# Optimization experiments

Measured on AMD Instinct MI355X. Metric: run time of the kernel, lower is better.

Reference implementation:

```python
import jax, jax.numpy as jnp
import numpy as np
from jax import lax

B, M = 16384, 128
NUM_LAYERS, OW, OH = 22, 11, 11
MAX_VEC = np.array([9.0, 1.0, 1.0, 10.0, 3.0, 254.0, 1.0, 1.0, 235.0, 8.0, 9.0, 250.0,
                    29.0, 1.0, 1.0, 8.0, 1.0, 1.0, 6.0, 3.0, 1.0, 2.0], dtype=np.float32)


def setup_inputs() -> dict:
    key = jax.random.key(0)
    ks = jax.random.split(key, 20)
    s = 0.05
    return {
        "observations": jax.random.randint(ks[0], (B, M, 3), 0, 255, dtype=jnp.int32),
        "cnn1_w": jax.random.normal(ks[1], (64, 22, 5, 5), jnp.float32) * s,
        "cnn1_b": jnp.zeros((64,), jnp.float32),
        "cnn2_w": jax.random.normal(ks[2], (64, 64, 3, 3), jnp.float32) * s,
        "cnn2_b": jnp.zeros((64,), jnp.float32),
        "fc1_w": jax.random.normal(ks[3], (128, 64), jnp.float32) * s,
        "fc1_b": jnp.zeros((128,), jnp.float32),
        "enc_w": jax.random.normal(ks[4], (128, 128), jnp.float32) * s,
        "enc_b": jnp.zeros((128,), jnp.float32),
        "critic1_w": jax.random.normal(ks[5], (1024, 128), jnp.float32) * s,
        "critic1_b": jnp.zeros((1024,), jnp.float32),
        "value_w": jax.random.normal(ks[6], (1, 1024), jnp.float32) * s,
        "value_b": jnp.zeros((1,), jnp.float32),
        "actor1_w": jax.random.normal(ks[7], (512, 128), jnp.float32) * s,
        "actor1_b": jnp.zeros((512,), jnp.float32),
        "action_emb": jax.random.normal(ks[8], (100, 16), jnp.float32) * s,
        "head0_w": jax.random.normal(ks[9], (9, 528), jnp.float32) * s,
        "head0_b": jnp.zeros((9,), jnp.float32),
        "head1_w": jax.random.normal(ks[10], (10, 528), jnp.float32) * s,
        "head1_b": jnp.zeros((10,), jnp.float32),
    }


def _encode_scatter(observations):
    # zero-out any byte equal to 255 (matches torch in-place masking)
    tok = jnp.where(observations == 255, 0, observations)  # [B, M, 3]
    coords = tok[..., 0].astype(jnp.uint8)
    x = ((coords >> 4) & 15).astype(jnp.int32)
    y = (coords & 15).astype(jnp.int32)
    atr = tok[..., 1].astype(jnp.int32)
    val = tok[..., 2].astype(jnp.float32)
    b, m = atr.shape
    valid = (x < OW) & (y < OH) & (atr < NUM_LAYERS)
    b_idx = jnp.broadcast_to(jnp.arange(b, dtype=jnp.int32)[:, None], (b, m))
    b_idx = jnp.where(valid, b_idx, b)  # route invalid tokens out of bounds -> dropped
    box = jnp.zeros((b, NUM_LAYERS, OW, OH), jnp.float32)
    box = box.at[b_idx, atr, x, y].set(val, mode="drop")
    return box


def _forward(observations, cnn1_w, cnn1_b, cnn2_w, cnn2_b, fc1_w, fc1_b, enc_w, enc_b,
             critic1_w, critic1_b, value_w, value_b, actor1_w, actor1_b, action_emb,
             head0_w, head0_b, head1_w, head1_b):
    box = _encode_scatter(observations)
    x = box / jnp.asarray(MAX_VEC)[None, :, None, None]
    dn = ("NCHW", "OIHW", "NCHW")
    x = lax.conv_general_dilated(x, cnn1_w, (3, 3), "VALID", dimension_numbers=dn) + cnn1_b[None, :, None, None]
    x = lax.conv_general_dilated(x, cnn2_w, (1, 1), "VALID", dimension_numbers=dn) + cnn2_b[None, :, None, None]
    x = x.reshape(x.shape[0], -1)                 # [B, 64]
    x = x @ fc1_w.T + fc1_b                       # [B, 128]
    hidden = x @ enc_w.T + enc_b                  # [B, 128]
    critic = jnp.tanh(hidden @ critic1_w.T + critic1_b)
    value = critic @ value_w.T + value_b          # [B, 1]
    actor = hidden @ actor1_w.T + actor1_b        # [B, 512]
    emb = jnp.broadcast_to(action_emb.mean(axis=0)[None, :], (actor.shape[0], action_emb.shape[1]))
    comb = jnp.concatenate([actor, emb], axis=-1)  # [B, 528]
    logits = jnp.concatenate([comb @ head0_w.T + head0_b, comb @ head1_w.T + head1_b], axis=-1)
    return logits, value


def reference(observations, cnn1_w, cnn1_b, cnn2_w, cnn2_b, fc1_w, fc1_b, enc_w, enc_b,
              critic1_w, critic1_b, value_w, value_b, actor1_w, actor1_b, action_emb,
              head0_w, head0_b, head1_w, head1_b):
    return _forward(observations, cnn1_w, cnn1_b, cnn2_w, cnn2_b, fc1_w, fc1_b, enc_w, enc_b,
                    critic1_w, critic1_b, value_w, value_b, actor1_w, actor1_b, action_emb,
                    head0_w, head0_b, head1_w, head1_b)
```

## Files before the change

### kernel.cpp

```cpp
#include <hip/hip_runtime.h>
#include <math.h>

#define NB 16384
#define NTOK 128
#define NKEY 2662
#define NLOG 19
#define TB 16

typedef __attribute__((ext_vector_type(8))) short short8;
typedef __attribute__((ext_vector_type(4))) float floatx4;

__device__ __constant__ float c_maxv[22] = {
    9.f, 1.f, 1.f, 10.f, 3.f, 254.f, 1.f, 1.f, 235.f, 8.f, 9.f, 250.f,
    29.f, 1.f, 1.f, 8.f, 1.f, 1.f, 6.f, 3.f, 1.f, 2.f};

__device__ __forceinline__ unsigned short f2bf(float f) {
    unsigned u = __float_as_uint(f);
    return (unsigned short)((u + 0x7FFFu + ((u >> 16) & 1u)) >> 16);
}
__device__ __forceinline__ float tanh_fast(float x) {
    float e = __builtin_amdgcn_exp2f(x * 2.885390082f);
    return 1.f - 2.f * __builtin_amdgcn_rcpf(e + 1.f);
}

__global__ __launch_bounds__(256) void k_pre(
    const float* __restrict__ w1, const float* __restrict__ b1,
    const float* __restrict__ w2, const float* __restrict__ b2,
    const float* __restrict__ fc1w, const float* __restrict__ fc1b,
    const float* __restrict__ encw, const float* __restrict__ encb,
    const float* __restrict__ a1w, const float* __restrict__ a1b,
    const float* __restrict__ aemb,
    const float* __restrict__ h0w, const float* __restrict__ h0b,
    const float* __restrict__ h1w, const float* __restrict__ h1b,
    const float* __restrict__ c1w,
    float* __restrict__ G, float* __restrict__ E,
    float* __restrict__ beff, float* __restrict__ Wlog,
    float* __restrict__ blog, unsigned short* __restrict__ c1wb)
{
    __shared__ float s_w2[72 * 65];
    __shared__ float s_h2[64];
    __shared__ float s_t[128];
    __shared__ float s_emb[16];
    const int bid = blockIdx.x, t = threadIdx.x;
    if (bid < 666) {
        const int v = t & 63;
        const int key_u = __builtin_amdgcn_readfirstlane(bid * 4 + (t >> 6));
        const int key_c = (key_u < NKEY) ? key_u : (NKEY - 1);
        const int c = key_c / 121, rem = key_c % 121, X = rem / 11, Y = rem % 11;
        float acc = 0.f;
        for (int u0 = 0; u0 < 64; u0 += 8) {
            __syncthreads();
            #pragma unroll
            for (int r = 0; r < 18; ++r) {
                int g = t + 256 * r;
                int vg = g / 72, rg = g % 72;
                s_w2[rg * 65 + vg] = w2[vg * 576 + u0 * 9 + rg];
            }
            __syncthreads();
            #pragma unroll
            for (int ur = 0; ur < 8; ++ur) {
                const int w1base = (u0 + ur) * 550 + c * 25;
                #pragma unroll
                for (int i = 0; i < 3; ++i) {
                    int xi = X - 3 * i;
                    if (xi < 0 || xi > 4) continue;
                    #pragma unroll
                    for (int j = 0; j < 3; ++j) {
                        int yj = Y - 3 * j;
                        if (yj < 0 || yj > 4) continue;
                        acc += s_w2[(ur * 9 + i * 3 + j) * 65 + v] *
                               w1[w1base + xi * 5 + yj];
                    }
                }
            }
        }
        if (key_u < NKEY) G[key_u * 64 + v] = acc / c_maxv[c];
    } else if (bid < 698) {
        int m = (bid - 666) * 256 + t;
        int h = __builtin_amdgcn_readfirstlane(m >> 6) & 127;
        int v = t & 63;
        float acc = 0.f;
        #pragma unroll 8
        for (int p = 0; p < 128; ++p)
            acc += encw[h * 128 + p] * fc1w[p * 64 + v];
        E[v * 128 + h] = acc;
    } else if (bid == 698) {
        {
            int o = t >> 2, q = t & 3;
            const float* wp = w2 + (o * 64 + q * 16) * 9;
            float s = 0.f;
            #pragma unroll
            for (int ui = 0; ui < 16; ++ui) {
                float ws = 0.f;
                #pragma unroll
                for (int k = 0; k < 9; ++k) ws += wp[ui * 9 + k];
                s += b1[q * 16 + ui] * ws;
            }
            s += __shfl_xor(s, 1, 64);
            s += __shfl_xor(s, 2, 64);
            if (q == 0) s_h2[o] = s + b2[o];
        }
        __syncthreads();
        if (t < 128) {
            const float4* f4 = (const float4*)(fc1w + t * 64);
            float s = fc1b[t];
            #pragma unroll
            for (int vq = 0; vq < 16; ++vq) {
                float4 w = f4[vq];
                s += w.x * s_h2[vq * 4]     + w.y * s_h2[vq * 4 + 1] +
                     w.z * s_h2[vq * 4 + 2] + w.w * s_h2[vq * 4 + 3];
            }
            s_t[t] = s;
        } else if (t < 192) {
            int lane = t & 63;
            int e = lane & 15, rq = lane >> 4;
            float s = 0.f;
            #pragma unroll
            for (int rr = 0; rr < 25; ++rr) s += aemb[(rq * 25 + rr) * 16 + e];
            s += __shfl_xor(s, 16, 64);
            s += __shfl_xor(s, 32, 64);
            if (lane < 16) s_emb[e] = s * 0.01f;
        }
        __syncthreads();
        if (t < 128) {
            const float4* e4 = (const float4*)(encw + t * 128);
            float s = encb[t];
            #pragma unroll
            for (int pq = 0; pq < 32; ++pq) {
                float4 w = e4[pq];
                s += w.x * s_t[pq * 4]     + w.y * s_t[pq * 4 + 1] +
                     w.z * s_t[pq * 4 + 2] + w.w * s_t[pq * 4 + 3];
            }
            beff[t] = s;
        } else {
            int tp = t - 128;
            int os = tp >> 3, ai = tp & 7;
            #pragma unroll
            for (int rep = 0; rep < 2; ++rep) {
                int o = os + rep * 16;
                int oc = (o < NLOG) ? o : (NLOG - 1);
                const float* hw = (oc < 9) ? (h0w + oc * 528)
                                           : (h1w + (oc - 9) * 528);
                float s = 0.f;
                for (int a = ai; a < 528; a += 8) {
                    float m = (a < 512) ? a1b[a] : s_emb[a - 512];
                    s += hw[a] * m;
                }
                s += __shfl_xor(s, 1, 64);
                s += __shfl_xor(s, 2, 64);
                s += __shfl_xor(s, 4, 64);
                if (ai == 0 && o < NLOG)
                    blog[o] = s + ((o < 9) ? h0b[o] : h1b[o - 9]);
            }
        }
    } else if (bid < 709) {
        int n = (bid - 699) * 256 + t;
        if (n < NLOG * 128) {
            int o = __builtin_amdgcn_readfirstlane(n >> 7);
            int h = n & 127;
            const float* hw = (o < 9) ? (h0w + o * 528) : (h1w + (o - 9) * 528);
            float acc = 0.f;
            #pragma unroll 8
            for (int a = 0; a < 512; ++a)
                acc += hw[a] * a1w[a * 128 + h];
            Wlog[n] = acc;
        }
    } else {
        int n = ((bid - 709) * 256 + t) * 8;
        float4 a = *(const float4*)(c1w + n);
        float4 b4 = *(const float4*)(c1w + n + 4);
        short8 r;
        r[0] = (short)f2bf(a.x);  r[1] = (short)f2bf(a.y);
        r[2] = (short)f2bf(a.z);  r[3] = (short)f2bf(a.w);
        r[4] = (short)f2bf(b4.x); r[5] = (short)f2bf(b4.y);
        r[6] = (short)f2bf(b4.z); r[7] = (short)f2bf(b4.w);
        *(short8*)(c1wb + n) = r;
    }
}

__global__ __launch_bounds__(512, 6) void k_main(
    const int* __restrict__ obs,
    const float* __restrict__ G, const float* __restrict__ E,
    const float* __restrict__ beff,
    const unsigned short* __restrict__ c1wb, const float* __restrict__ c1b,
    const float* __restrict__ vw, const float* __restrict__ vb,
    const float* __restrict__ Wlog, const float* __restrict__ blog,
    float* __restrict__ out)
{
    __shared__ int            s_lst[TB * 32];
    __shared__ float          s_hidden[TB * 128];
    __shared__ unsigned short s_hb[TB * 136];
    __shared__ float          s_x[TB * 64];
    __shared__ int            s_cnt[TB];
    __shared__ float          s_val[8 * 16];

    const int tid = threadIdx.x, bid = blockIdx.x;
    const int b0 = bid * TB;

    if (tid < TB) s_cnt[tid] = 0;
    __syncthreads();

    {
        const int4* p = (const int4*)(obs + (size_t)(b0 * NTOK + 4 * tid) * 3);
        int4 A = p[0], Bv = p[1], Cv = p[2];
        int d[12] = {A.x, A.y, A.z, A.w, Bv.x, Bv.y, Bv.z, Bv.w,
                     Cv.x, Cv.y, Cv.z, Cv.w};
        #pragma unroll
        for (int s = 0; s < 4; ++s) {
            int o0 = d[3 * s], o1 = d[3 * s + 1], o2 = d[3 * s + 2];
            o0 = (o0 == 255) ? 0 : o0;
            o1 = (o1 == 255) ? 0 : o1;
            o2 = (o2 == 255) ? 0 : o2;
            int x = (o0 >> 4) & 15, y = o0 & 15;
            if (x < 11 && y < 11 && o1 < 22) {
                int tt = 4 * tid + s;
                int bb = tt >> 7, m = tt & 127;
                int pos = atomicAdd(&s_cnt[bb], 1);
                if (pos < 32)
                    s_lst[bb * 32 + pos] =
                        (m << 20) | (o2 << 12) | (o1 * 121 + x * 11 + y);
            }
        }
    }
    __syncthreads();

    {
        int bb = tid >> 5, e = tid & 31;
        int n = s_cnt[bb]; if (n > 32) n = 32;
        if (e < n) {
            int p = s_lst[bb * 32 + e];
            bool dead = false;
            for (int i = 0; i < n; ++i) {
                int q = s_lst[bb * 32 + i];
                dead |= (((q ^ p) & 0xFFF) == 0) && (q > p);
            }
            if (dead) s_lst[bb * 32 + e] = p & ~0x000FF000;
        }
    }
    __syncthreads();

    {
        int w = tid >> 6, lane = tid & 63;
        int bbA = 2 * w, bbB = 2 * w + 1;
        int nA = s_cnt[bbA]; if (nA > 32) nA = 32;
        int nB = s_cnt[bbB]; if (nB > 32) nB = 32;
        int nm = (nA > nB) ? nA : nB;
        float aA = 0.f, aB = 0.f;
        for (int i = 0; i < nm; ++i) {
            if (i < nA) {
                int p = s_lst[bbA * 32 + i];
                aA += (float)((p >> 12) & 0xFF) * G[(p & 0xFFF) * 64 + lane];
            }
            if (i < nB) {
                int p = s_lst[bbB * 32 + i];
                aB += (float)((p >> 12) & 0xFF) * G[(p & 0xFFF) * 64 + lane];
            }
        }
        s_x[bbA * 64 + lane] = aA;
        s_x[bbB * 64 + lane] = aB;
    }
    __syncthreads();

    {
        int g = tid >> 7, h = tid & 127;
        float be = beff[h];
        float acc[4] = {be, be, be, be};
        const float4* x4 = (const float4*)s_x;
        #pragma unroll
        for (int vq = 0; vq < 16; ++vq) {
            float ev0 = E[(vq * 4 + 0) * 128 + h];
            float ev1 = E[(vq * 4 + 1) * 128 + h];
            float ev2 = E[(vq * 4 + 2) * 128 + h];
            float ev3 = E[(vq * 4 + 3) * 128 + h];
            #pragma unroll
            for (int b = 0; b < 4; ++b) {
                float4 xv = x4[(g * 4 + b) * 16 + vq];
                acc[b] += xv.x * ev0 + xv.y * ev1 + xv.z * ev2 + xv.w * ev3;
            }
        }
        #pragma unroll
        for (int b = 0; b < 4; ++b) {
            int bb = g * 4 + b;
            s_hidden[bb * 128 + h] = acc[b];
            s_hb[bb * 136 + h] = f2bf(acc[b]);
        }
    }
    __syncthreads();

    {
        const int lane = tid & 63, w = tid >> 6;
        const int lm = lane & 15, quad = lane >> 4;
        short8 af[4];
        #pragma unroll
        for (int kk = 0; kk < 4; ++kk)
            af[kk] = *(const short8*)&s_hb[lm * 136 + kk * 32 + quad * 8];
        float vp[4] = {0.f, 0.f, 0.f, 0.f};
        for (int nt = 0; nt < 8; ++nt) {
            int j = w * 128 + nt * 16 + lm;
            const short8* cp = (const short8*)&c1wb[j * 128];
            floatx4 a0 = {0.f, 0.f, 0.f, 0.f};
            #pragma unroll
            for (int kk = 0; kk < 4; ++kk) {
                short8 bf = cp[kk * 4 + quad];
                a0 = __builtin_amdgcn_mfma_f32_16x16x32_bf16(af[kk], bf, a0, 0, 0, 0);
            }
            float bj = c1b[j], wj = vw[j];
            #pragma unroll
            for (int r = 0; r < 4; ++r)
                vp[r] += tanh_fast(a0[r] + bj) * wj;
        }
        #pragma unroll
        for (int off = 1; off <= 8; off <<= 1)
            #pragma unroll
            for (int r = 0; r < 4; ++r)
                vp[r] += __shfl_xor(vp[r], off, 64);
        if (lm == 0) {
            #pragma unroll
            for (int r = 0; r < 4; ++r)
                s_val[w * 16 + quad * 4 + r] = vp[r];
        }
    }

    {
        const float4* s_h4 = (const float4*)s_hidden;
        const float4* wl4  = (const float4*)Wlog;
        int bl = tid >> 5, o = tid & 31;
        if (o < NLOG) {
            float acc = blog[o];
            #pragma unroll
            for (int hq = 0; hq < 32; ++hq) {
                float4 hv = s_h4[bl * 32 + hq];
                float4 wl = wl4[o * 32 + hq];
                acc += wl.x * hv.x + wl.y * hv.y + wl.z * hv.z + wl.w * hv.w;
            }
            out[(b0 + bl) * NLOG + o] = acc;
        }
    }
    __syncthreads();
    if (tid < TB) {
        float v = 0.f;
        #pragma unroll
        for (int w = 0; w < 8; ++w) v += s_val[w * 16 + tid];
        out[NB * NLOG + b0 + tid] = v + vb[0];
    }
}

extern "C" void kernel_launch(void* const* d_in, const int* in_sizes, int n_in,
                              void* d_out, int out_size, void* d_ws, size_t ws_size,
                              hipStream_t stream)
{
    const int*   obs  = (const int*)  d_in[0];
    const float* w1   = (const float*)d_in[1];
    const float* b1   = (const float*)d_in[2];
    const float* w2   = (const float*)d_in[3];
    const float* b2   = (const float*)d_in[4];
    const float* fc1w = (const float*)d_in[5];
    const float* fc1b = (const float*)d_in[6];
    const float* encw = (const float*)d_in[7];
    const float* encb = (const float*)d_in[8];
    const float* c1w  = (const float*)d_in[9];
    const float* c1b  = (const float*)d_in[10];
    const float* vw   = (const float*)d_in[11];
    const float* vb   = (const float*)d_in[12];
    const float* a1w  = (const float*)d_in[13];
    const float* a1b  = (const float*)d_in[14];
    const float* aemb = (const float*)d_in[15];
    const float* h0w  = (const float*)d_in[16];
    const float* h0b  = (const float*)d_in[17];
    const float* h1w  = (const float*)d_in[18];
    const float* h1b  = (const float*)d_in[19];

    float* W    = (float*)d_ws;
    float* G    = W;
    float* E    = W + 170368;
    float* beff = W + 178560;
    float* Wlog = W + 178688;
    float* blog = W + 181120;
    unsigned short* c1wb = (unsigned short*)(W + 181152);

    hipLaunchKernelGGL(k_pre, dim3(773), dim3(256), 0, stream,
                       w1, b1, w2, b2, fc1w, fc1b, encw, encb, a1w, a1b, aemb,
                       h0w, h0b, h1w, h1b, c1w,
                       G, E, beff, Wlog, blog, c1wb);
    hipLaunchKernelGGL(k_main, dim3(NB / TB), dim3(512), 0, stream,
                       obs, G, E, beff, c1wb, c1b, vw, vb, Wlog, blog,
                       (float*)d_out);
}
```

Before: 200.1 us.

## Enlarge main-kernel batch tile to 64 and compute 4 keys per wave in precompute

The main kernel now handles 64 batch rows per block with 1024 threads. Each wave computes four 16-row MFMA tiles against the same bf16 critic weight fragments, so every weight load is reused four times and global weight traffic per row drops. The precompute kernel gives each wave four G keys so the staged conv2 weights in shared memory are reused more, which cuts its block count. The cost is a quarter as many main blocks (256), more registers per thread, and lower occupancy limits.

```diff
diff --git a/kernel.cpp b/kernel.cpp
--- a/kernel.cpp
+++ b/kernel.cpp
@@ -5,7 +5,7 @@
 #define NTOK 128
 #define NKEY 2662
 #define NLOG 19
-#define TB 16
+#define TB 64
 
 typedef __attribute__((ext_vector_type(8))) short short8;
 typedef __attribute__((ext_vector_type(4))) float floatx4;
@@ -42,12 +42,19 @@
     __shared__ float s_t[128];
     __shared__ float s_emb[16];
     const int bid = blockIdx.x, t = threadIdx.x;
-    if (bid < 666) {
+    if (bid < 167) {
         const int v = t & 63;
-        const int key_u = __builtin_amdgcn_readfirstlane(bid * 4 + (t >> 6));
-        const int key_c = (key_u < NKEY) ? key_u : (NKEY - 1);
-        const int c = key_c / 121, rem = key_c % 121, X = rem / 11, Y = rem % 11;
-        float acc = 0.f;
+        const int wv = __builtin_amdgcn_readfirstlane(t >> 6);
+        int c_[4], X_[4], Y_[4];
+        #pragma unroll
+        for (int kk = 0; kk < 4; ++kk) {
+            int key_u = bid * 16 + wv * 4 + kk;
+            int key_c = (key_u < NKEY) ? key_u : (NKEY - 1);
+            c_[kk] = key_c / 121;
+            int rem = key_c % 121;
+            X_[kk] = rem / 11; Y_[kk] = rem % 11;
+        }
+        float acc[4] = {0.f, 0.f, 0.f, 0.f};
         for (int u0 = 0; u0 < 64; u0 += 8) {
             __syncthreads();
             #pragma unroll
@@ -59,24 +66,32 @@
             __syncthreads();
             #pragma unroll
             for (int ur = 0; ur < 8; ++ur) {
-                const int w1base = (u0 + ur) * 550 + c * 25;
                 #pragma unroll
-                for (int i = 0; i < 3; ++i) {
-                    int xi = X - 3 * i;
-                    if (xi < 0 || xi > 4) continue;
+                for (int kk = 0; kk < 4; ++kk) {
+                    const int w1base = (u0 + ur) * 550 + c_[kk] * 25;
                     #pragma unroll
-                    for (int j = 0; j < 3; ++j) {
-                        int yj = Y - 3 * j;
-                        if (yj < 0 || yj > 4) continue;
-                        acc += s_w2[(ur * 9 + i * 3 + j) * 65 + v] *
-                               w1[w1base + xi * 5 + yj];
+                    for (int i = 0; i < 3; ++i) {
+                        int xi = X_[kk] - 3 * i;
+                        if (xi < 0 || xi > 4) continue;
+                        #pragma unroll
+                        for (int j = 0; j < 3; ++j) {
+                            int yj = Y_[kk] - 3 * j;
+                            if (yj < 0 || yj > 4) continue;
+                            acc[kk] += s_w2[(ur * 9 + i * 3 + j) * 65 + v] *
+                                       w1[w1base + xi * 5 + yj];
+                        }
                     }
                 }
             }
         }
-        if (key_u < NKEY) G[key_u * 64 + v] = acc / c_maxv[c];
-    } else if (bid < 698) {
-        int m = (bid - 666) * 256 + t;
+        #pragma unroll
+        for (int kk = 0; kk < 4; ++kk) {
+            int key_u = bid * 16 + wv * 4 + kk;
+            if (key_u < NKEY)
+                G[key_u * 64 + v] = acc[kk] / c_maxv[c_[kk]];
+        }
+    } else if (bid < 199) {
+        int m = (bid - 167) * 256 + t;
         int h = __builtin_amdgcn_readfirstlane(m >> 6) & 127;
         int v = t & 63;
         float acc = 0.f;
@@ -84,7 +99,7 @@
         for (int p = 0; p < 128; ++p)
             acc += encw[h * 128 + p] * fc1w[p * 64 + v];
         E[v * 128 + h] = acc;
-    } else if (bid == 698) {
+    } else if (bid == 199) {
         {
             int o = t >> 2, q = t & 3;
             const float* wp = w2 + (o * 64 + q * 16) * 9;
@@ -153,8 +168,8 @@
                     blog[o] = s + ((o < 9) ? h0b[o] : h1b[o - 9]);
             }
         }
-    } else if (bid < 709) {
-        int n = (bid - 699) * 256 + t;
+    } else if (bid < 210) {
+        int n = (bid - 200) * 256 + t;
         if (n < NLOG * 128) {
             int o = __builtin_amdgcn_readfirstlane(n >> 7);
             int h = n & 127;
@@ -166,7 +181,7 @@
             Wlog[n] = acc;
         }
     } else {
-        int n = ((bid - 709) * 256 + t) * 8;
+        int n = ((bid - 210) * 256 + t) * 8;
         float4 a = *(const float4*)(c1w + n);
         float4 b4 = *(const float4*)(c1w + n + 4);
         short8 r;
@@ -178,7 +193,7 @@
     }
 }
 
-__global__ __launch_bounds__(512, 6) void k_main(
+__global__ __launch_bounds__(1024, 4) void k_main(
     const int* __restrict__ obs,
     const float* __restrict__ G, const float* __restrict__ E,
     const float* __restrict__ beff,
@@ -192,7 +207,7 @@
     __shared__ unsigned short s_hb[TB * 136];
     __shared__ float          s_x[TB * 64];
     __shared__ int            s_cnt[TB];
-    __shared__ float          s_val[8 * 16];
+    __shared__ float          s_val[16 * 64];
 
     const int tid = threadIdx.x, bid = blockIdx.x;
     const int b0 = bid * TB;
@@ -201,70 +216,82 @@
     __syncthreads();
 
     {
-        const int4* p = (const int4*)(obs + (size_t)(b0 * NTOK + 4 * tid) * 3);
-        int4 A = p[0], Bv = p[1], Cv = p[2];
-        int d[12] = {A.x, A.y, A.z, A.w, Bv.x, Bv.y, Bv.z, Bv.w,
-                     Cv.x, Cv.y, Cv.z, Cv.w};
-        #pragma unroll
-        for (int s = 0; s < 4; ++s) {
-            int o0 = d[3 * s], o1 = d[3 * s + 1], o2 = d[3 * s + 2];
-            o0 = (o0 == 255) ? 0 : o0;
-            o1 = (o1 == 255) ? 0 : o1;
-            o2 = (o2 == 255) ? 0 : o2;
-            int x = (o0 >> 4) & 15, y = o0 & 15;
-            if (x < 11 && y < 11 && o1 < 22) {
-                int tt = 4 * tid + s;
-                int bb = tt >> 7, m = tt & 127;
-                int pos = atomicAdd(&s_cnt[bb], 1);
-                if (pos < 32)
-                    s_lst[bb * 32 + pos] =
-                        (m << 20) | (o2 << 12) | (o1 * 121 + x * 11 + y);
-            }
-        }
-    }
-    __syncthreads();
-
-    {
-        int bb = tid >> 5, e = tid & 31;
-        int n = s_cnt[bb]; if (n > 32) n = 32;
-        if (e < n) {
-            int p = s_lst[bb * 32 + e];
-            bool dead = false;
-            for (int i = 0; i < n; ++i) {
-                int q = s_lst[bb * 32 + i];
-                dead |= (((q ^ p) & 0xFFF) == 0) && (q > p);
-            }
-            if (dead) s_lst[bb * 32 + e] = p & ~0x000FF000;
+        const int gtok0 = b0 * NTOK;
+        #pragma unroll
+        for (int k = 0; k < 2; ++k) {
+            int g = tid + 1024 * k;
+            const int4* p = (const int4*)(obs + (size_t)(gtok0 + 4 * g) * 3);
+            int4 A = p[0], Bv = p[1], Cv = p[2];
+            int d[12] = {A.x, A.y, A.z, A.w, Bv.x, Bv.y, Bv.z, Bv.w,
+                         Cv.x, Cv.y, Cv.z, Cv.w};
+            #pragma unroll
+            for (int s = 0; s < 4; ++s) {
+                int o0 = d[3 * s], o1 = d[3 * s + 1], o2 = d[3 * s + 2];
+                o0 = (o0 == 255) ? 0 : o0;
+                o1 = (o1 == 255) ? 0 : o1;
+                o2 = (o2 == 255) ? 0 : o2;
+                int x = (o0 >> 4) & 15, y = o0 & 15;
+                if (x < 11 && y < 11 && o1 < 22) {
+                    int tt = 4 * g + s;
+                    int bb = tt >> 7, m = tt & 127;
+                    int pos = atomicAdd(&s_cnt[bb], 1);
+                    if (pos < 32)
+                        s_lst[bb * 32 + pos] =
+                            (m << 20) | (o2 << 12) | (o1 * 121 + x * 11 + y);
+                }
+            }
+        }
+    }
+    __syncthreads();
+
+    {
+        #pragma unroll
+        for (int rep = 0; rep < 2; ++rep) {
+            int bb = (tid >> 5) + rep * 32, e = tid & 31;
+            int n = s_cnt[bb]; if (n > 32) n = 32;
+            if (e < n) {
+                int p = s_lst[bb * 32 + e];
+                bool dead = false;
+                for (int i = 0; i < n; ++i) {
+                    int q = s_lst[bb * 32 + i];
+                    dead |= (((q ^ p) & 0xFFF) == 0) && (q > p);
+                }
+                if (dead) s_lst[bb * 32 + e] = p & ~0x000FF000;
+            }
         }
     }
     __syncthreads();
 
     {
         int w = tid >> 6, lane = tid & 63;
-        int bbA = 2 * w, bbB = 2 * w + 1;
-        int nA = s_cnt[bbA]; if (nA > 32) nA = 32;
-        int nB = s_cnt[bbB]; if (nB > 32) nB = 32;
-        int nm = (nA > nB) ? nA : nB;
-        float aA = 0.f, aB = 0.f;
+        int n4[4], nm = 0;
+        #pragma unroll
+        for (int q = 0; q < 4; ++q) {
+            int n = s_cnt[w * 4 + q]; if (n > 32) n = 32;
+            n4[q] = n; nm = (n > nm) ? n : nm;
+        }
+        float a4[4] = {0.f, 0.f, 0.f, 0.f};
         for (int i = 0; i < nm; ++i) {
-            if (i < nA) {
-                int p = s_lst[bbA * 32 + i];
-                aA += (float)((p >> 12) & 0xFF) * G[(p & 0xFFF) * 64 + lane];
-            }
-            if (i < nB) {
-                int p = s_lst[bbB * 32 + i];
-                aB += (float)((p >> 12) & 0xFF) * G[(p & 0xFFF) * 64 + lane];
-            }
-        }
-        s_x[bbA * 64 + lane] = aA;
-        s_x[bbB * 64 + lane] = aB;
+            #pragma unroll
+            for (int q = 0; q < 4; ++q) {
+                if (i < n4[q]) {
+                    int p = s_lst[(w * 4 + q) * 32 + i];
+                    a4[q] += (float)((p >> 12) & 0xFF) * G[(p & 0xFFF) * 64 + lane];
+                }
+            }
+        }
+        #pragma unroll
+        for (int q = 0; q < 4; ++q)
+            s_x[(w * 4 + q) * 64 + lane] = a4[q];
     }
     __syncthreads();
 
     {
         int g = tid >> 7, h = tid & 127;
         float be = beff[h];
-        float acc[4] = {be, be, be, be};
+        float acc[8];
+        #pragma unroll
+        for (int b = 0; b < 8; ++b) acc[b] = be;
         const float4* x4 = (const float4*)s_x;
         #pragma unroll
         for (int vq = 0; vq < 16; ++vq) {
@@ -273,14 +300,14 @@
             float ev2 = E[(vq * 4 + 2) * 128 + h];
             float ev3 = E[(vq * 4 + 3) * 128 + h];
             #pragma unroll
-            for (int b = 0; b < 4; ++b) {
-                float4 xv = x4[(g * 4 + b) * 16 + vq];
+            for (int b = 0; b < 8; ++b) {
+                float4 xv = x4[(g * 8 + b) * 16 + vq];
                 acc[b] += xv.x * ev0 + xv.y * ev1 + xv.z * ev2 + xv.w * ev3;
             }
         }
         #pragma unroll
-        for (int b = 0; b < 4; ++b) {
-            int bb = g * 4 + b;
+        for (int b = 0; b < 8; ++b) {
+            int bb = g * 8 + b;
             s_hidden[bb * 128 + h] = acc[b];
             s_hb[bb * 136 + h] = f2bf(acc[b]);
         }
@@ -290,57 +317,80 @@
     {
         const int lane = tid & 63, w = tid >> 6;
         const int lm = lane & 15, quad = lane >> 4;
-        short8 af[4];
-        #pragma unroll
-        for (int kk = 0; kk < 4; ++kk)
-            af[kk] = *(const short8*)&s_hb[lm * 136 + kk * 32 + quad * 8];
-        float vp[4] = {0.f, 0.f, 0.f, 0.f};
-        for (int nt = 0; nt < 8; ++nt) {
-            int j = w * 128 + nt * 16 + lm;
+        short8 af[4][4];
+        #pragma unroll
+        for (int mt = 0; mt < 4; ++mt)
+            #pragma unroll
+            for (int kk = 0; kk < 4; ++kk)
+                af[mt][kk] = *(const short8*)
+                    &s_hb[(mt * 16 + lm) * 136 + kk * 32 + quad * 8];
+        float vp[4][4];
+        #pragma unroll
+        for (int mt = 0; mt < 4; ++mt)
+            #pragma unroll
+            for (int r = 0; r < 4; ++r) vp[mt][r] = 0.f;
+        #pragma unroll
+        for (int nt = 0; nt < 4; ++nt) {
+            int j = w * 64 + nt * 16 + lm;
             const short8* cp = (const short8*)&c1wb[j * 128];
-            floatx4 a0 = {0.f, 0.f, 0.f, 0.f};
+            floatx4 a0 = {0.f,0.f,0.f,0.f}, a1 = {0.f,0.f,0.f,0.f};
+            floatx4 a2 = {0.f,0.f,0.f,0.f}, a3 = {0.f,0.f,0.f,0.f};
             #pragma unroll
             for (int kk = 0; kk < 4; ++kk) {
                 short8 bf = cp[kk * 4 + quad];
-                a0 = __builtin_amdgcn_mfma_f32_16x16x32_bf16(af[kk], bf, a0, 0, 0, 0);
+                a0 = __builtin_amdgcn_mfma_f32_16x16x32_bf16(af[0][kk], bf, a0, 0, 0, 0);
+                a1 = __builtin_amdgcn_mfma_f32_16x16x32_bf16(af[1][kk], bf, a1, 0, 0, 0);
+                a2 = __builtin_amdgcn_mfma_f32_16x16x32_bf16(af[2][kk], bf, a2, 0, 0, 0);
+                a3 = __builtin_amdgcn_mfma_f32_16x16x32_bf16(af[3][kk], bf, a3, 0, 0, 0);
             }
             float bj = c1b[j], wj = vw[j];
             #pragma unroll
-            for (int r = 0; r < 4; ++r)
-                vp[r] += tanh_fast(a0[r] + bj) * wj;
+            for (int r = 0; r < 4; ++r) {
+                vp[0][r] += tanh_fast(a0[r] + bj) * wj;
+                vp[1][r] += tanh_fast(a1[r] + bj) * wj;
+                vp[2][r] += tanh_fast(a2[r] + bj) * wj;
+                vp[3][r] += tanh_fast(a3[r] + bj) * wj;
+            }
         }
         #pragma unroll
         for (int off = 1; off <= 8; off <<= 1)
             #pragma unroll
-            for (int r = 0; r < 4; ++r)
-                vp[r] += __shfl_xor(vp[r], off, 64);
+            for (int mt = 0; mt < 4; ++mt)
+                #pragma unroll
+                for (int r = 0; r < 4; ++r)
+                    vp[mt][r] += __shfl_xor(vp[mt][r], off, 64);
         if (lm == 0) {
             #pragma unroll
-            for (int r = 0; r < 4; ++r)
-                s_val[w * 16 + quad * 4 + r] = vp[r];
+            for (int mt = 0; mt < 4; ++mt)
+                #pragma unroll
+                for (int r = 0; r < 4; ++r)
+                    s_val[w * 64 + mt * 16 + quad * 4 + r] = vp[mt][r];
         }
     }
 
     {
         const float4* s_h4 = (const float4*)s_hidden;
         const float4* wl4  = (const float4*)Wlog;
-        int bl = tid >> 5, o = tid & 31;
-        if (o < NLOG) {
-            float acc = blog[o];
-            #pragma unroll
-            for (int hq = 0; hq < 32; ++hq) {
-                float4 hv = s_h4[bl * 32 + hq];
-                float4 wl = wl4[o * 32 + hq];
-                acc += wl.x * hv.x + wl.y * hv.y + wl.z * hv.z + wl.w * hv.w;
-            }
-            out[(b0 + bl) * NLOG + o] = acc;
+        #pragma unroll
+        for (int rep = 0; rep < 2; ++rep) {
+            int bl = (tid >> 5) + rep * 32, o = tid & 31;
+            if (o < NLOG) {
+                float acc = blog[o];
+                #pragma unroll
+                for (int hq = 0; hq < 32; ++hq) {
+                    float4 hv = s_h4[bl * 32 + hq];
+                    float4 wl = wl4[o * 32 + hq];
+                    acc += wl.x * hv.x + wl.y * hv.y + wl.z * hv.z + wl.w * hv.w;
+                }
+                out[(b0 + bl) * NLOG + o] = acc;
+            }
         }
     }
     __syncthreads();
     if (tid < TB) {
         float v = 0.f;
         #pragma unroll
-        for (int w = 0; w < 8; ++w) v += s_val[w * 16 + tid];
+        for (int w = 0; w < 16; ++w) v += s_val[w * 64 + tid];
         out[NB * NLOG + b0 + tid] = v + vb[0];
     }
 }
@@ -378,11 +428,11 @@
     float* blog = W + 181120;
     unsigned short* c1wb = (unsigned short*)(W + 181152);
 
-    hipLaunchKernelGGL(k_pre, dim3(773), dim3(256), 0, stream,
+    hipLaunchKernelGGL(k_pre, dim3(274), dim3(256), 0, stream,
                        w1, b1, w2, b2, fc1w, fc1b, encw, encb, a1w, a1b, aemb,
                        h0w, h0b, h1w, h1b, c1w,
                        G, E, beff, Wlog, blog, c1wb);
-    hipLaunchKernelGGL(k_main, dim3(NB / TB), dim3(512), 0, stream,
+    hipLaunchKernelGGL(k_main, dim3(NB / TB), dim3(1024), 0, stream,
                        obs, G, E, beff, c1wb, c1b, vw, vb, Wlog, blog,
                        (float*)d_out);
 }
```

New measurement: 242.9 us. +21.4%, slower.

## Double batch tile per block and reuse critic weight fragments across two MFMAs

Applied to the files above, without the earlier changes.

Raises the per-block batch tile from 16 to 32 rows and the block size from 512 to 1024 threads. In the critic layer each wave now covers 64 output columns and runs two MFMAs, one per 16-row half, that share each loaded bf16 weight fragment. This halves how often the critic weight matrix is re-read from cache across the grid. In exchange, occupancy limits change to two 1024-thread blocks per CU, register budgets tighten, and A fragments are now reloaded from LDS inside the loop instead of being held in registers.

```diff
diff --git a/kernel.cpp b/kernel.cpp
--- a/kernel.cpp
+++ b/kernel.cpp
@@ -5,7 +5,7 @@
 #define NTOK 128
 #define NKEY 2662
 #define NLOG 19
-#define TB 16
+#define TB 32
 
 typedef __attribute__((ext_vector_type(8))) short short8;
 typedef __attribute__((ext_vector_type(4))) float floatx4;
@@ -178,7 +178,7 @@
     }
 }
 
-__global__ __launch_bounds__(512, 6) void k_main(
+__global__ __launch_bounds__(1024, 2) void k_main(
     const int* __restrict__ obs,
     const float* __restrict__ G, const float* __restrict__ E,
     const float* __restrict__ beff,
@@ -192,7 +192,7 @@
     __shared__ unsigned short s_hb[TB * 136];
     __shared__ float          s_x[TB * 64];
     __shared__ int            s_cnt[TB];
-    __shared__ float          s_val[8 * 16];
+    __shared__ float          s_val[16 * 32];
 
     const int tid = threadIdx.x, bid = blockIdx.x;
     const int b0 = bid * TB;
@@ -290,34 +290,41 @@
     {
         const int lane = tid & 63, w = tid >> 6;
         const int lm = lane & 15, quad = lane >> 4;
-        short8 af[4];
-        #pragma unroll
-        for (int kk = 0; kk < 4; ++kk)
-            af[kk] = *(const short8*)&s_hb[lm * 136 + kk * 32 + quad * 8];
-        float vp[4] = {0.f, 0.f, 0.f, 0.f};
-        for (int nt = 0; nt < 8; ++nt) {
-            int j = w * 128 + nt * 16 + lm;
+        float vp0[4] = {0.f, 0.f, 0.f, 0.f}, vp1[4] = {0.f, 0.f, 0.f, 0.f};
+        #pragma unroll
+        for (int nt = 0; nt < 4; ++nt) {
+            int j = w * 64 + nt * 16 + lm;
             const short8* cp = (const short8*)&c1wb[j * 128];
-            floatx4 a0 = {0.f, 0.f, 0.f, 0.f};
+            floatx4 a0 = {0.f, 0.f, 0.f, 0.f}, a1 = {0.f, 0.f, 0.f, 0.f};
             #pragma unroll
             for (int kk = 0; kk < 4; ++kk) {
-                short8 bf = cp[kk * 4 + quad];
-                a0 = __builtin_amdgcn_mfma_f32_16x16x32_bf16(af[kk], bf, a0, 0, 0, 0);
+                short8 bf  = cp[kk * 4 + quad];
+                short8 af0 = *(const short8*)&s_hb[lm * 136 + kk * 32 + quad * 8];
+                short8 af1 = *(const short8*)&s_hb[(16 + lm) * 136 + kk * 32 + quad * 8];
+                a0 = __builtin_amdgcn_mfma_f32_16x16x32_bf16(af0, bf, a0, 0, 0, 0);
+                a1 = __builtin_amdgcn_mfma_f32_16x16x32_bf16(af1, bf, a1, 0, 0, 0);
             }
             float bj = c1b[j], wj = vw[j];
             #pragma unroll
-            for (int r = 0; r < 4; ++r)
-                vp[r] += tanh_fast(a0[r] + bj) * wj;
-        }
-        #pragma unroll
-        for (int off = 1; off <= 8; off <<= 1)
-            #pragma unroll
-            for (int r = 0; r < 4; ++r)
-                vp[r] += __shfl_xor(vp[r], off, 64);
+            for (int r = 0; r < 4; ++r) {
+                vp0[r] += tanh_fast(a0[r] + bj) * wj;
+                vp1[r] += tanh_fast(a1[r] + bj) * wj;
+            }
+        }
+        #pragma unroll
+        for (int off = 1; off <= 8; off <<= 1) {
+            #pragma unroll
+            for (int r = 0; r < 4; ++r) {
+                vp0[r] += __shfl_xor(vp0[r], off, 64);
+                vp1[r] += __shfl_xor(vp1[r], off, 64);
+            }
+        }
         if (lm == 0) {
             #pragma unroll
-            for (int r = 0; r < 4; ++r)
-                s_val[w * 16 + quad * 4 + r] = vp[r];
+            for (int r = 0; r < 4; ++r) {
+                s_val[w * 32 + quad * 4 + r]      = vp0[r];
+                s_val[w * 32 + 16 + quad * 4 + r] = vp1[r];
+            }
         }
     }
 
@@ -340,7 +347,7 @@
     if (tid < TB) {
         float v = 0.f;
         #pragma unroll
-        for (int w = 0; w < 8; ++w) v += s_val[w * 16 + tid];
+        for (int w = 0; w < 16; ++w) v += s_val[w * 32 + tid];
         out[NB * NLOG + b0 + tid] = v + vb[0];
     }
 }
@@ -382,7 +389,7 @@
                        w1, b1, w2, b2, fc1w, fc1b, encw, encb, a1w, a1b, aemb,
                        h0w, h0b, h1w, h1b, c1w,
                        G, E, beff, Wlog, blog, c1wb);
-    hipLaunchKernelGGL(k_main, dim3(NB / TB), dim3(512), 0, stream,
+    hipLaunchKernelGGL(k_main, dim3(NB / TB), dim3(1024), 0, stream,
                        obs, G, E, beff, c1wb, c1b, vw, vb, Wlog, blog,
                        (float*)d_out);
 }
```

New measurement: 196.2 us. -2.0%, faster.
